# Kernel optimization log

Hardware: AMD Instinct MI355X
Metric: run time of the kernel (lower is better)

The kernel has to match this reference:

```python
import jax, jax.numpy as jnp
import numpy as np

CLIP_RATIO = 0.9  # input_clip_ratio from __init__
QMAX = 7.0        # int4 symmetric: values in [-8, 7]


def setup_inputs() -> dict:
    key = jax.random.key(0)
    x = jax.random.normal(key, (4, 2048, 4096), dtype=jnp.float32)
    return {"x": x}


def reference(x):
    # Per-token (last-dim) symmetric int4 quantization with clip ratio, then bit-pack.
    absmax = jnp.max(jnp.abs(x), axis=-1, keepdims=True)          # [B, S, 1]
    scales = absmax * CLIP_RATIO / QMAX                            # [B, S, 1]
    scales = jnp.maximum(scales, jnp.float32(1e-8))                # avoid div-by-zero
    q = jnp.clip(jnp.round(x / scales), -8.0, 7.0).astype(jnp.int32)  # int4 range
    # Pack two int4 values per byte: element 0 -> low nibble, element 1 -> high nibble.
    qu = (q & 0xF).astype(jnp.uint8)                               # two's-complement nibble
    packed = ((qu[..., 1::2] << 4) | qu[..., 0::2]).astype(jnp.int8)  # [B, S, H//2]
    return packed, scales
```

## Files before the change

kernel.cpp:

```cpp
#include <hip/hip_runtime.h>

#define H 4096
#define BLOCK 256
#define PER_THREAD (H / BLOCK)
#define VECS (PER_THREAD / 4)

__global__ __launch_bounds__(BLOCK) void quant_int4_kernel(
    const float* __restrict__ x,
    float* __restrict__ out_packed,
    float* __restrict__ out_scales,
    float r7)
{
    const int row = blockIdx.x;
    const int t = threadIdx.x;
    const float4* xr = reinterpret_cast<const float4*>(x + (size_t)row * H);

    float4 v[VECS];
    float m = 0.0f;
#pragma unroll
    for (int j = 0; j < VECS; ++j) {
        v[j] = xr[t + BLOCK * j];
        m = fmaxf(m, fmaxf(fmaxf(fabsf(v[j].x), fabsf(v[j].y)),
                           fmaxf(fabsf(v[j].z), fabsf(v[j].w))));
    }

#pragma unroll
    for (int off = 32; off > 0; off >>= 1)
        m = fmaxf(m, __shfl_xor(m, off, 64));

    __shared__ float smax[BLOCK / 64];
    const int wave = t >> 6;
    if ((t & 63) == 0) smax[wave] = m;
    __syncthreads();
    if (t == 0) {
        float mm = smax[0];
#pragma unroll
        for (int w = 1; w < BLOCK / 64; ++w) mm = fmaxf(mm, smax[w]);
        smax[0] = mm;
    }
    __syncthreads();
    const float absmax = smax[0];

    float tt = absmax * 0.9f;
    asm volatile("" : "+v"(tt));
    float s = tt * r7;
    s = fmaxf(s, 1e-8f);

    double s64 = (double)s;
    asm volatile("" : "+v"(s64));
    double inv = 1.0 / s64;
    inv = inv * (2.0 - s64 * inv);
    asm volatile("" : "+v"(inv));

    float2* outp = reinterpret_cast<float2*>(out_packed + (size_t)row * (H / 2));
#pragma unroll
    for (int j = 0; j < VECS; ++j) {
        float qf0 = (float)((double)v[j].x * inv);
        float qf1 = (float)((double)v[j].y * inv);
        float qf2 = (float)((double)v[j].z * inv);
        float qf3 = (float)((double)v[j].w * inv);
        int q0 = (int)rintf(qf0); q0 = max(-8, min(7, q0));
        int q1 = (int)rintf(qf1); q1 = max(-8, min(7, q1));
        int q2 = (int)rintf(qf2); q2 = max(-8, min(7, q2));
        int q3 = (int)rintf(qf3); q3 = max(-8, min(7, q3));
        int b0 = ((q1 & 0xF) << 4) | (q0 & 0xF);
        int b1 = ((q3 & 0xF) << 4) | (q2 & 0xF);
        float f0 = (float)(signed char)(b0 & 0xFF);
        float f1 = (float)(signed char)(b1 & 0xFF);
        outp[t + BLOCK * j] = make_float2(f0, f1);
    }

    if (t == 0) out_scales[row] = s;
}

extern "C" void kernel_launch(void* const* d_in, const int* in_sizes, int n_in,
                              void* d_out, int out_size, void* d_ws, size_t ws_size,
                              hipStream_t stream) {
    const float* x = (const float*)d_in[0];
    const int n = in_sizes[0];
    const int rows = n / H;
    float* out = (float*)d_out;
    float* out_packed = out;
    float* out_scales = out + (size_t)n / 2;

    const float r7 = 1.0f / 7.0f;
    quant_int4_kernel<<<rows, BLOCK, 0, stream>>>(x, out_packed, out_scales, r7);
}
```

Baseline: 34.49 us.

## Use 512-thread blocks with two contiguous float4 loads and one float4 store per thread

Doubles the block size to 512 threads so each thread handles 8 contiguous elements: two adjacent 16-byte loads and one 16-byte store of four packed outputs, replacing four strided loads and four 8-byte stores. This widens the stores and gives more waves per row, which should raise occupancy and memory-level parallelism. In exchange, each thread's two loads now cover 32 contiguous bytes instead of fully coalesced 16-byte strides across the wave. The reduction also now spans 8 waves, adding a little shared-memory work.

```diff
diff --git a/kernel.cpp b/kernel.cpp
--- a/kernel.cpp
+++ b/kernel.cpp
@@ -1,9 +1,10 @@
 #include <hip/hip_runtime.h>
 
 #define H 4096
-#define BLOCK 256
+#define BLOCK 512
 #define PER_THREAD (H / BLOCK)
-#define VECS (PER_THREAD / 4)
+
+typedef float f32x4 __attribute__((ext_vector_type(4)));
 
 __global__ __launch_bounds__(BLOCK) void quant_int4_kernel(
     const float* __restrict__ x,
@@ -13,16 +14,14 @@
 {
     const int row = blockIdx.x;
     const int t = threadIdx.x;
-    const float4* xr = reinterpret_cast<const float4*>(x + (size_t)row * H);
+    const f32x4* xr = reinterpret_cast<const f32x4*>(x + (size_t)row * H);
 
-    float4 v[VECS];
-    float m = 0.0f;
-#pragma unroll
-    for (int j = 0; j < VECS; ++j) {
-        v[j] = xr[t + BLOCK * j];
-        m = fmaxf(m, fmaxf(fmaxf(fabsf(v[j].x), fabsf(v[j].y)),
-                           fmaxf(fabsf(v[j].z), fabsf(v[j].w))));
-    }
+    f32x4 va = xr[2 * t];
+    f32x4 vb = xr[2 * t + 1];
+    float m = fmaxf(fmaxf(fmaxf(fabsf(va.x), fabsf(va.y)),
+                          fmaxf(fabsf(va.z), fabsf(va.w))),
+                    fmaxf(fmaxf(fabsf(vb.x), fabsf(vb.y)),
+                          fmaxf(fabsf(vb.z), fabsf(vb.w))));
 
 #pragma unroll
     for (int off = 32; off > 0; off >>= 1)
@@ -52,23 +51,29 @@
     inv = inv * (2.0 - s64 * inv);
     asm volatile("" : "+v"(inv));
 
-    float2* outp = reinterpret_cast<float2*>(out_packed + (size_t)row * (H / 2));
-#pragma unroll
-    for (int j = 0; j < VECS; ++j) {
-        float qf0 = (float)((double)v[j].x * inv);
-        float qf1 = (float)((double)v[j].y * inv);
-        float qf2 = (float)((double)v[j].z * inv);
-        float qf3 = (float)((double)v[j].w * inv);
-        int q0 = (int)rintf(qf0); q0 = max(-8, min(7, q0));
-        int q1 = (int)rintf(qf1); q1 = max(-8, min(7, q1));
-        int q2 = (int)rintf(qf2); q2 = max(-8, min(7, q2));
-        int q3 = (int)rintf(qf3); q3 = max(-8, min(7, q3));
-        int b0 = ((q1 & 0xF) << 4) | (q0 & 0xF);
-        int b1 = ((q3 & 0xF) << 4) | (q2 & 0xF);
-        float f0 = (float)(signed char)(b0 & 0xFF);
-        float f1 = (float)(signed char)(b1 & 0xFF);
-        outp[t + BLOCK * j] = make_float2(f0, f1);
-    }
+    f32x4* outp = reinterpret_cast<f32x4*>(out_packed + (size_t)row * (H / 2));
+    float qa0 = (float)((double)va.x * inv);
+    float qa1 = (float)((double)va.y * inv);
+    float qa2 = (float)((double)va.z * inv);
+    float qa3 = (float)((double)va.w * inv);
+    float qb0 = (float)((double)vb.x * inv);
+    float qb1 = (float)((double)vb.y * inv);
+    float qb2 = (float)((double)vb.z * inv);
+    float qb3 = (float)((double)vb.w * inv);
+    int a0 = (int)rintf(qa0); a0 = max(-8, min(7, a0));
+    int a1 = (int)rintf(qa1); a1 = max(-8, min(7, a1));
+    int a2 = (int)rintf(qa2); a2 = max(-8, min(7, a2));
+    int a3 = (int)rintf(qa3); a3 = max(-8, min(7, a3));
+    int b0 = (int)rintf(qb0); b0 = max(-8, min(7, b0));
+    int b1 = (int)rintf(qb1); b1 = max(-8, min(7, b1));
+    int b2 = (int)rintf(qb2); b2 = max(-8, min(7, b2));
+    int b3 = (int)rintf(qb3); b3 = max(-8, min(7, b3));
+    f32x4 o;
+    o.x = (float)(signed char)((((a1 & 0xF) << 4) | (a0 & 0xF)) & 0xFF);
+    o.y = (float)(signed char)((((a3 & 0xF) << 4) | (a2 & 0xF)) & 0xFF);
+    o.z = (float)(signed char)((((b1 & 0xF) << 4) | (b0 & 0xF)) & 0xFF);
+    o.w = (float)(signed char)((((b3 & 0xF) << 4) | (b2 & 0xF)) & 0xFF);
+    outp[t] = o;
 
     if (t == 0) out_scales[row] = s;
 }
```

Measured after the change: 33.91 us. No clear change (-1.7%).
